# Kernel tuning notes

Measured on AMD Instinct MI355X. Metric: run time of the kernel, lower is better.

## Reference

```python
import jax, jax.numpy as jnp
import numpy as np

EPS = 1e-12  # torch F.normalize eps

def _l2norm(x):
    n = jnp.sqrt(jnp.sum(x * x, axis=-1, keepdims=True))
    return x / jnp.maximum(n, EPS)

def setup_inputs() -> dict:
    key = jax.random.key(0)
    k1, k2 = jax.random.split(key)
    B, C, H, W = 4, 256, 48, 48
    qkv = jax.random.normal(k1, (B, 3 * C, H, W), dtype=jnp.float32)
    temp = jnp.ones((8, 1, 1), dtype=jnp.float32)
    proj_w = jax.random.normal(k2, (C, C), dtype=jnp.float32) * (1.0 / np.sqrt(C))
    proj_b = jnp.zeros((C,), dtype=jnp.float32)
    return {"qkv": qkv, "temp": temp, "proj_w": proj_w, "proj_b": proj_b, "h": H, "w": W}

def reference(qkv, temp, proj_w, proj_b, h, w):
    num_heads = temp.shape[0]
    b = qkv.shape[0]
    q, k, v = jnp.split(qkv, 3, axis=1)

    def to_heads(x):
        # b (head c) h w -> b head (h w) c
        return x.reshape(b, num_heads, -1, h * w).transpose(0, 1, 3, 2)

    q = _l2norm(to_heads(q))
    k = _l2norm(to_heads(k))
    v = to_heads(v)

    # [b, head, N, N], temp (head,1,1) broadcasts over (n, m)
    attn = jnp.einsum('bhnc,bhmc->bhnm', q, k) * temp
    attn = jax.nn.softmax(jax.nn.relu(attn), axis=-1)
    out = jnp.einsum('bhnm,bhmc->bhnc', attn, v)
    # b head N c -> b head c N -> b (head c) h w
    out = out.transpose(0, 1, 3, 2).reshape(b, -1, h, w)
    # 1x1 conv == channel matmul
    out = jnp.einsum('oc,bchw->bohw', proj_w, out) + proj_b[None, :, None, None]
    return out
```

## Files before the change

### kernel.cpp

```cpp
#include <hip/hip_runtime.h>

typedef unsigned short u16;
typedef unsigned int   u32;
typedef __attribute__((ext_vector_type(8))) short short8;
typedef __attribute__((ext_vector_type(4))) float f32x4;

#define NB    4
#define NCH   256
#define NHD   8
#define HD    32
#define NSP   2304
#define NBH   32
#define NKT   36
#define KPW   18

__device__ __forceinline__ u16 f2bf(float f) {
    u32 u = __float_as_uint(f);
    u += 0x7FFFu + ((u >> 16) & 1u);
    return (u16)(u >> 16);
}
__device__ __forceinline__ u32 pack2(float a, float b) {
    return (u32)f2bf(a) | ((u32)f2bf(b) << 16);
}
__device__ __forceinline__ u32 pkfast(float a, float b) {
#if __has_builtin(__builtin_amdgcn_cvt_pk_bf16_f32)
    typedef __attribute__((ext_vector_type(2))) __bf16 bf2;
    union { bf2 v; u32 u; } cv;
    cv.v = __builtin_amdgcn_cvt_pk_bf16_f32(a, b);
    return cv.u;
#else
    return __builtin_amdgcn_perm(__float_as_uint(b), __float_as_uint(a), 0x07060302u);
#endif
}
__device__ __forceinline__ float fexp2(float x) {
#if __has_builtin(__builtin_amdgcn_exp2f)
    return __builtin_amdgcn_exp2f(x);
#else
    return exp2f(x);
#endif
}

__global__ __launch_bounds__(256) void wcast_kernel(const float* __restrict__ w,
                                                    u16* __restrict__ wb) {
    int i = blockIdx.x * 256 + threadIdx.x;
    float4 v = ((const float4*)w)[i];
    ((uint2*)wb)[i] = make_uint2(pack2(v.x, v.y), pack2(v.z, v.w));
}

__global__ __launch_bounds__(64) void prep_kernel(
    const float* __restrict__ qkv, const float* __restrict__ temp,
    u16* __restrict__ Qn, u16* __restrict__ Kn, u16* __restrict__ Vp)
{
    const int p  = blockIdx.y;
    const int bh = blockIdx.z, b = bh >> 3, head = bh & 7;
    const int n  = blockIdx.x * 64 + threadIdx.x;
    const float* src = qkv + ((size_t)(b * 3 * NCH + p * NCH + head * HD)) * NSP + n;

    float v[HD];
#pragma unroll
    for (int d = 0; d < HD; ++d) v[d] = src[(size_t)d * NSP];

    if (p == 2) {
        const int loc = threadIdx.x, c = loc >> 5, r5 = loc & 31;
        const int qd  = (r5 < 16) ? (r5 >> 2) : ((r5 - 16) >> 2);
        const int jj  = (r5 < 16) ? (r5 & 3) : (4 + (r5 & 3));
        u16* dst = Vp + (size_t)bh * NSP * HD + (size_t)blockIdx.x * 2048 + c * 32 + qd * 8 + jj;
#pragma unroll
        for (int d = 0; d < HD; ++d) dst[d * 64] = f2bf(v[d]);
    } else {
        float s = 0.f;
#pragma unroll
        for (int d = 0; d < HD; ++d) s += v[d] * v[d];
        float sc = 1.f / fmaxf(sqrtf(s), 1e-12f);
        if (p == 0) sc *= temp[head] * 1.44269504088896f;
        u32 pk[HD / 2];
#pragma unroll
        for (int i = 0; i < HD / 2; ++i) pk[i] = pack2(v[2 * i] * sc, v[2 * i + 1] * sc);
        u16* dst = (p == 0 ? Qn : Kn) + ((size_t)bh * NSP + n) * HD;
#pragma unroll
        for (int i = 0; i < 4; ++i) ((uint4*)dst)[i] = ((const uint4*)pk)[i];
    }
}

__global__ __launch_bounds__(128) void attn_kernel(
    const u16* __restrict__ Qn, const u16* __restrict__ Kn,
    const u16* __restrict__ Vp, u16* __restrict__ X)
{
    __shared__ float cmb[64][25];
    const int bh = blockIdx.y, b = bh >> 3, head = bh & 7;
    const int w = threadIdx.x >> 6, lane = threadIdx.x & 63;
    const int l15 = lane & 15, quad = lane >> 4;
    const int qbase = blockIdx.x * 32;

    const u16* Kg = Kn + (size_t)bh * NSP * HD + (size_t)w * KPW * 2048 + l15 * HD + quad * 8;
    const u16* Vg = Vp + (size_t)bh * NSP * HD + (size_t)w * KPW * 2048 + l15 * 64 + quad * 8;

    short8 qfrag[2];
#pragma unroll
    for (int t2 = 0; t2 < 2; ++t2)
        qfrag[t2] = *(const short8*)(Qn + ((size_t)bh * NSP + qbase + t2 * 16 + l15) * HD + quad * 8);

    const short one = (short)0x3F80;
    const short8 vones = {one, one, one, one, one, one, one, one};

    f32x4 oacc[2][2] = {{{0,0,0,0},{0,0,0,0}},{{0,0,0,0},{0,0,0,0}}};
    f32x4 rsac[2]    = {{0,0,0,0},{0,0,0,0}};

    for (int kt = 0; kt < KPW; ++kt) {
        short8 ka[4], vbf[2][2];
#pragma unroll
        for (int i = 0; i < 4; ++i)
            ka[i] = *(const short8*)(Kg + i * 512);
#pragma unroll
        for (int c = 0; c < 2; ++c)
#pragma unroll
            for (int h = 0; h < 2; ++h)
                vbf[c][h] = *(const short8*)(Vg + h * 1024 + c * 32);
        Kg += 2048; Vg += 2048;

#pragma unroll
        for (int t2 = 0; t2 < 2; ++t2) {
            f32x4 sf[4];
#pragma unroll
            for (int i = 0; i < 4; ++i)
                sf[i] = __builtin_amdgcn_mfma_f32_16x16x32_bf16(ka[i], qfrag[t2], (f32x4){0.f,0.f,0.f,0.f}, 0, 0, 0);
            u32 pk[4][2];
#pragma unroll
            for (int i = 0; i < 4; ++i) {
                pk[i][0] = pkfast(fexp2(fmaxf(sf[i][0], 0.f)), fexp2(fmaxf(sf[i][1], 0.f)));
                pk[i][1] = pkfast(fexp2(fmaxf(sf[i][2], 0.f)), fexp2(fmaxf(sf[i][3], 0.f)));
            }
#pragma unroll
            for (int c = 0; c < 2; ++c) {
                union { short8 s; u32 u[4]; } pa;
                pa.u[0] = pk[2 * c][0];     pa.u[1] = pk[2 * c][1];
                pa.u[2] = pk[2 * c + 1][0]; pa.u[3] = pk[2 * c + 1][1];
                oacc[t2][0] = __builtin_amdgcn_mfma_f32_16x16x32_bf16(pa.s, vbf[c][0], oacc[t2][0], 0, 0, 0);
                oacc[t2][1] = __builtin_amdgcn_mfma_f32_16x16x32_bf16(pa.s, vbf[c][1], oacc[t2][1], 0, 0, 0);
                rsac[t2]    = __builtin_amdgcn_mfma_f32_16x16x32_bf16(pa.s, vones,     rsac[t2],    0, 0, 0);
            }
        }
    }

    if (w == 1) {
#pragma unroll
        for (int t2 = 0; t2 < 2; ++t2) {
#pragma unroll
            for (int h = 0; h < 2; ++h)
#pragma unroll
                for (int r = 0; r < 4; ++r) cmb[lane][t2 * 8 + h * 4 + r] = oacc[t2][h][r];
#pragma unroll
            for (int r = 0; r < 4; ++r) cmb[lane][16 + t2 * 4 + r] = rsac[t2][r];
        }
    }
    __syncthreads();
    if (w == 0) {
        u16* Xb = X + (size_t)b * NSP * NCH + head * HD;
#pragma unroll
        for (int t2 = 0; t2 < 2; ++t2) {
            float inv[4];
#pragma unroll
            for (int r = 0; r < 4; ++r)
                inv[r] = 1.f / (rsac[t2][r] + cmb[lane][16 + t2 * 4 + r]);
#pragma unroll
            for (int r = 0; r < 4; ++r) {
                u16* row = Xb + (size_t)(qbase + t2 * 16 + quad * 4 + r) * NCH;
                row[l15]      = f2bf((oacc[t2][0][r] + cmb[lane][t2 * 8 + r])     * inv[r]);
                row[16 + l15] = f2bf((oacc[t2][1][r] + cmb[lane][t2 * 8 + 4 + r]) * inv[r]);
            }
        }
    }
}

__global__ __launch_bounds__(64) void proj_kernel(
    const u16* __restrict__ Wb, const u16* __restrict__ X,
    const float* __restrict__ bias, float* __restrict__ out)
{
    const int b = blockIdx.z;
    const int lane = threadIdx.x;
    const int l15 = lane & 15, quad = lane >> 4;
    const int obase = blockIdx.y * 16;
    const int nbase = blockIdx.x * 32;

    const u16* wrow = Wb + (size_t)(obase + l15) * NCH + quad * 8;
    const u16* xrow = X + ((size_t)b * NSP + nbase + l15) * NCH + quad * 8;

    f32x4 acc[2] = {{0,0,0,0},{0,0,0,0}};
#pragma unroll
    for (int ks = 0; ks < 8; ++ks) {
        const short8 af = *(const short8*)(wrow + ks * 32);
        acc[0] = __builtin_amdgcn_mfma_f32_16x16x32_bf16(af, *(const short8*)(xrow + ks * 32), acc[0], 0, 0, 0);
        acc[1] = __builtin_amdgcn_mfma_f32_16x16x32_bf16(af, *(const short8*)(xrow + (size_t)16 * NCH + ks * 32), acc[1], 0, 0, 0);
    }
#pragma unroll
    for (int r = 0; r < 4; ++r) {
        const int o = obase + quad * 4 + r;
        const float bo = bias[o];
        float* orow = out + ((size_t)b * NCH + o) * NSP + nbase;
        orow[l15]      = acc[0][r] + bo;
        orow[16 + l15] = acc[1][r] + bo;
    }
}

extern "C" void kernel_launch(void* const* d_in, const int* in_sizes, int n_in,
                              void* d_out, int out_size, void* d_ws, size_t ws_size,
                              hipStream_t stream) {
    const float* qkv   = (const float*)d_in[0];
    const float* temp  = (const float*)d_in[1];
    const float* projw = (const float*)d_in[2];
    const float* projb = (const float*)d_in[3];
    float* out = (float*)d_out;

    u16* Qn = (u16*)d_ws;
    u16* Kn = Qn + (size_t)NBH * NSP * HD;
    u16* Vp = Kn + (size_t)NBH * NSP * HD;
    u16* X  = Vp + (size_t)NBH * NSP * HD;
    u16* Wb = X + (size_t)NB * NSP * NCH;

    wcast_kernel<<<dim3(64), dim3(256), 0, stream>>>(projw, Wb);
    prep_kernel<<<dim3(NSP / 64, 3, NBH), dim3(64), 0, stream>>>(qkv, temp, Qn, Kn, Vp);
    attn_kernel<<<dim3(NSP / 32, NBH), dim3(128), 0, stream>>>(Qn, Kn, Vp, X);
    proj_kernel<<<dim3(NSP / 32, NCH / 16, NB), dim3(64), 0, stream>>>(Wb, X, projb, out);
}
```

Before: 165.1 us.

## Split attention key range over four waves with register prefetch and swapped grid order

```diff
diff --git a/kernel.cpp b/kernel.cpp
--- a/kernel.cpp
+++ b/kernel.cpp
@@ -12,7 +12,7 @@
 #define NSP   2304
 #define NBH   32
 #define NKT   36
-#define KPW   18
+#define KPW   9
 
 __device__ __forceinline__ u16 f2bf(float f) {
     u32 u = __float_as_uint(f);
@@ -82,15 +82,15 @@
     }
 }
 
-__global__ __launch_bounds__(128) void attn_kernel(
+__global__ __launch_bounds__(256, 4) void attn_kernel(
     const u16* __restrict__ Qn, const u16* __restrict__ Kn,
     const u16* __restrict__ Vp, u16* __restrict__ X)
 {
-    __shared__ float cmb[64][25];
-    const int bh = blockIdx.y, b = bh >> 3, head = bh & 7;
+    __shared__ float cmb[3][64][25];
+    const int bh = blockIdx.x, b = bh >> 3, head = bh & 7;
     const int w = threadIdx.x >> 6, lane = threadIdx.x & 63;
     const int l15 = lane & 15, quad = lane >> 4;
-    const int qbase = blockIdx.x * 32;
+    const int qbase = blockIdx.y * 32;
 
     const u16* Kg = Kn + (size_t)bh * NSP * HD + (size_t)w * KPW * 2048 + l15 * HD + quad * 8;
     const u16* Vg = Vp + (size_t)bh * NSP * HD + (size_t)w * KPW * 2048 + l15 * 64 + quad * 8;
@@ -106,17 +106,26 @@
     f32x4 oacc[2][2] = {{{0,0,0,0},{0,0,0,0}},{{0,0,0,0},{0,0,0,0}}};
     f32x4 rsac[2]    = {{0,0,0,0},{0,0,0,0}};
 
+    short8 ka[4], vb[2][2];
+#pragma unroll
+    for (int i = 0; i < 4; ++i) ka[i] = *(const short8*)(Kg + i * 512);
+#pragma unroll
+    for (int c = 0; c < 2; ++c)
+#pragma unroll
+        for (int h = 0; h < 2; ++h) vb[c][h] = *(const short8*)(Vg + h * 1024 + c * 32);
+
     for (int kt = 0; kt < KPW; ++kt) {
-        short8 ka[4], vbf[2][2];
-#pragma unroll
-        for (int i = 0; i < 4; ++i)
-            ka[i] = *(const short8*)(Kg + i * 512);
-#pragma unroll
-        for (int c = 0; c < 2; ++c)
-#pragma unroll
-            for (int h = 0; h < 2; ++h)
-                vbf[c][h] = *(const short8*)(Vg + h * 1024 + c * 32);
-        Kg += 2048; Vg += 2048;
+        short8 kan[4], vbn[2][2];
+        if (kt + 1 < KPW) {
+            const u16* Kp2 = Kg + (size_t)(kt + 1) * 2048;
+            const u16* Vp2 = Vg + (size_t)(kt + 1) * 2048;
+#pragma unroll
+            for (int i = 0; i < 4; ++i) kan[i] = *(const short8*)(Kp2 + i * 512);
+#pragma unroll
+            for (int c = 0; c < 2; ++c)
+#pragma unroll
+                for (int h = 0; h < 2; ++h) vbn[c][h] = *(const short8*)(Vp2 + h * 1024 + c * 32);
+        }
 
 #pragma unroll
         for (int t2 = 0; t2 < 2; ++t2) {
@@ -135,22 +144,32 @@
                 union { short8 s; u32 u[4]; } pa;
                 pa.u[0] = pk[2 * c][0];     pa.u[1] = pk[2 * c][1];
                 pa.u[2] = pk[2 * c + 1][0]; pa.u[3] = pk[2 * c + 1][1];
-                oacc[t2][0] = __builtin_amdgcn_mfma_f32_16x16x32_bf16(pa.s, vbf[c][0], oacc[t2][0], 0, 0, 0);
-                oacc[t2][1] = __builtin_amdgcn_mfma_f32_16x16x32_bf16(pa.s, vbf[c][1], oacc[t2][1], 0, 0, 0);
-                rsac[t2]    = __builtin_amdgcn_mfma_f32_16x16x32_bf16(pa.s, vones,     rsac[t2],    0, 0, 0);
-            }
-        }
-    }
-
-    if (w == 1) {
+                oacc[t2][0] = __builtin_amdgcn_mfma_f32_16x16x32_bf16(pa.s, vb[c][0], oacc[t2][0], 0, 0, 0);
+                oacc[t2][1] = __builtin_amdgcn_mfma_f32_16x16x32_bf16(pa.s, vb[c][1], oacc[t2][1], 0, 0, 0);
+                rsac[t2]    = __builtin_amdgcn_mfma_f32_16x16x32_bf16(pa.s, vones,    rsac[t2],    0, 0, 0);
+            }
+        }
+
+        if (kt + 1 < KPW) {
+#pragma unroll
+            for (int i = 0; i < 4; ++i) ka[i] = kan[i];
+#pragma unroll
+            for (int c = 0; c < 2; ++c)
+#pragma unroll
+                for (int h = 0; h < 2; ++h) vb[c][h] = vbn[c][h];
+        }
+    }
+
+    if (w != 0) {
+        float* dst = &cmb[w - 1][lane][0];
 #pragma unroll
         for (int t2 = 0; t2 < 2; ++t2) {
 #pragma unroll
             for (int h = 0; h < 2; ++h)
 #pragma unroll
-                for (int r = 0; r < 4; ++r) cmb[lane][t2 * 8 + h * 4 + r] = oacc[t2][h][r];
-#pragma unroll
-            for (int r = 0; r < 4; ++r) cmb[lane][16 + t2 * 4 + r] = rsac[t2][r];
+                for (int r = 0; r < 4; ++r) dst[t2 * 8 + h * 4 + r] = oacc[t2][h][r];
+#pragma unroll
+            for (int r = 0; r < 4; ++r) dst[16 + t2 * 4 + r] = rsac[t2][r];
         }
     }
     __syncthreads();
@@ -158,15 +177,27 @@
         u16* Xb = X + (size_t)b * NSP * NCH + head * HD;
 #pragma unroll
         for (int t2 = 0; t2 < 2; ++t2) {
-            float inv[4];
-#pragma unroll
-            for (int r = 0; r < 4; ++r)
-                inv[r] = 1.f / (rsac[t2][r] + cmb[lane][16 + t2 * 4 + r]);
+            float o0[4], o1[4], rsum[4];
 #pragma unroll
             for (int r = 0; r < 4; ++r) {
+                o0[r] = oacc[t2][0][r]; o1[r] = oacc[t2][1][r]; rsum[r] = rsac[t2][r];
+            }
+#pragma unroll
+            for (int j = 0; j < 3; ++j) {
+                const float* srcp = &cmb[j][lane][0];
+#pragma unroll
+                for (int r = 0; r < 4; ++r) {
+                    o0[r]   += srcp[t2 * 8 + r];
+                    o1[r]   += srcp[t2 * 8 + 4 + r];
+                    rsum[r] += srcp[16 + t2 * 4 + r];
+                }
+            }
+#pragma unroll
+            for (int r = 0; r < 4; ++r) {
+                const float inv = 1.f / rsum[r];
                 u16* row = Xb + (size_t)(qbase + t2 * 16 + quad * 4 + r) * NCH;
-                row[l15]      = f2bf((oacc[t2][0][r] + cmb[lane][t2 * 8 + r])     * inv[r]);
-                row[16 + l15] = f2bf((oacc[t2][1][r] + cmb[lane][t2 * 8 + 4 + r]) * inv[r]);
+                row[l15]      = f2bf(o0[r] * inv);
+                row[16 + l15] = f2bf(o1[r] * inv);
             }
         }
     }
@@ -219,6 +250,6 @@
 
     wcast_kernel<<<dim3(64), dim3(256), 0, stream>>>(projw, Wb);
     prep_kernel<<<dim3(NSP / 64, 3, NBH), dim3(64), 0, stream>>>(qkv, temp, Qn, Kn, Vp);
-    attn_kernel<<<dim3(NSP / 32, NBH), dim3(128), 0, stream>>>(Qn, Kn, Vp, X);
+    attn_kernel<<<dim3(NBH, NSP / 32), dim3(256), 0, stream>>>(Qn, Kn, Vp, X);
     proj_kernel<<<dim3(NSP / 32, NCH / 16, NB), dim3(64), 0, stream>>>(Wb, X, projb, out);
 }
```

Result: faster. 159.3 us (-3.5%).
